# Kernel optimization log

Hardware: AMD Instinct MI355X
Metric: run time of the kernel (lower is better)

The kernel has to match this reference:

```python
import jax, jax.numpy as jnp
import numpy as np

B, NB, NS, C, HID, NP, NH = 8, 2048, 1024, 768, 3072, 1024, 6
HD = C // NH


def _ln(x, w, b):
    mu = x.mean(-1, keepdims=True)
    var = ((x - mu) ** 2).mean(-1, keepdims=True)
    return (x - mu) / jnp.sqrt(var + 1e-5) * w + b


def _gelu(z):
    return jax.nn.gelu(z, approximate=False)  # torch nn.GELU default = exact erf


def setup_inputs() -> dict:
    key = jax.random.key(0)
    ks = jax.random.split(key, 16)
    p = lambda i, shape: (jax.random.normal(ks[i], shape, jnp.float32) * 0.02)
    inp = {
        'x_b': jax.random.normal(ks[0], (B, NB, C), jnp.float32),
        'x_s': jax.random.normal(ks[1], (B, NS, C), jnp.float32),
        # token_types[0,0]=0 -> KV is computed (no stale cache), as on the first call
        'token_types': jax.random.randint(ks[2], (B, NS), 0, 2, jnp.int32).at[0, 0].set(0),
        'base_idxs': jax.random.randint(ks[3], (B, NP), -3, NB).astype(jnp.int32),
        'ln1_w': jnp.ones(C, jnp.float32), 'ln1_b': jnp.zeros(C, jnp.float32),
        'ln2_w': jnp.ones(C, jnp.float32), 'ln2_b': jnp.zeros(C, jnp.float32),
        'ln3_w': jnp.ones(C, jnp.float32), 'ln3_b': jnp.zeros(C, jnp.float32),
        'Wq': p(4, (C, C)), 'Wkv': p(5, (C, 2 * C)),
        'es_w1': p(6, (C, HID)), 'es_b1': jnp.zeros(HID, jnp.float32),
        'es_w2': p(7, (HID, C)), 'es_b2': jnp.zeros(C, jnp.float32),
        'el_w1': p(8, (C, HID)), 'el_b1': jnp.zeros(HID, jnp.float32),
        'el_w2': p(9, (HID, C)), 'el_b2': jnp.zeros(C, jnp.float32),
        'mlp_w1': p(10, (C, 4 * C)), 'mlp_b1': jnp.zeros(4 * C, jnp.float32),
        'mlp_w2': p(11, (4 * C, C)), 'mlp_b2': jnp.zeros(C, jnp.float32),
    }
    return inp


def reference(x_b, x_s, token_types, base_idxs,
              ln1_w, ln1_b, ln2_w, ln2_b, ln3_w, ln3_b,
              Wq, Wkv, es_w1, es_b1, es_w2, es_b2,
              el_w1, el_b1, el_w2, el_b2,
              mlp_w1, mlp_b1, mlp_w2, mlp_b2):
    Bn, Ns, Cd = x_s.shape
    # --- norm1/norm2 + cross-attention (q from x_s, kv from x_b) ---
    xs_n = _ln(x_s, ln1_w, ln1_b)
    xb_n = _ln(x_b, ln2_w, ln2_b)
    q = (xs_n @ Wq).reshape(Bn, Ns, NH, HD).transpose(0, 2, 1, 3)          # (B,H,Ns,hd)
    kv = (xb_n @ Wkv).reshape(Bn, -1, 2, NH, HD).transpose(2, 0, 3, 1, 4)  # (2,B,H,Nb,hd)
    k_, v_ = kv[0], kv[1]
    attn = jax.nn.softmax(jnp.einsum('bhqd,bhkd->bhqk', q, k_) * (HD ** -0.5), axis=-1)
    ctx = jnp.einsum('bhqk,bhkd->bhqd', attn, v_).transpose(0, 2, 1, 3).reshape(Bn, Ns, Cd)
    # --- 2-expert MoE MLP routed by token_types (0 -> expert_s, 1 -> expert_l) ---
    out_s = _gelu(ctx @ es_w1 + es_b1) @ es_w2 + es_b2
    out_l = _gelu(ctx @ el_w1 + el_b1) @ el_w2 + el_b2
    tt = token_types[..., None]
    moe = jnp.where(tt == 0, out_s, 0.0) + jnp.where(tt == 1, out_l, 0.0)
    x = x_s + moe
    # --- residual MLP ---
    x = x + (_gelu(_ln(x, ln3_w, ln3_b) @ mlp_w1 + mlp_b1) @ mlp_w2 + mlp_b2)
    x_norm = x / jnp.maximum(jnp.linalg.norm(x, axis=-1, keepdims=True), 1e-12)
    # --- masked-token kernel (vectorized over batch, masking replaces gather) ---
    nh = base_idxs.shape[1] // 2
    ids = base_idxs[:, :nh]
    mask = ids >= 0                                        # (B,nh)
    idc = jnp.where(mask, ids, 0)
    tokens = jnp.take_along_axis(x_b, idc[:, :, None], axis=1) * mask[..., None]
    sc = jnp.einsum('bic,bjc->bij', tokens, tokens) / jnp.sqrt(jnp.float32(Cd))
    kbias = jnp.where(mask, 0.0, -1e9)[:, None, :]
    aw = jax.nn.softmax(sc + kbias, axis=-1)
    agg = jnp.einsum('bij,bjc->bic', aw, tokens)
    cnt = mask.sum(-1)
    ksum = (agg * mask[..., None]).sum(1) / jnp.maximum(cnt, 1)[:, None]
    kn = ksum / jnp.maximum(jnp.linalg.norm(ksum, axis=-1, keepdims=True), 1e-12)
    has = (cnt > 0)[:, None]
    kernel = jnp.where(has, kn, 0.0)                        # (B,C)
    pos = jnp.where(has, (jnp.einsum('bnc,bc->bn', x_norm, kernel) + 1.0) / 2.0, 0.0)
    # --- top-k selection with data-dependent valid_k and straight-through binarize ---
    kk = Ns // 8
    topv, topi = jax.lax.top_k(pos, kk)
    cnt65 = (pos > 0.65).sum(-1)
    vk = jnp.minimum(kk, jnp.maximum(kk - 10, cnt65))
    keep = jnp.arange(kk)[None, :] < vk[:, None]
    vals = topv * keep
    sel = vals[:, :, None] * jax.nn.one_hot(topi, Ns, dtype=x.dtype)
    binary = (sel > 0.0).astype(x.dtype)
    sel = sel + jax.lax.stop_gradient(binary - sel)
    return sel, topi, pos, x, kernel[:, None, :]
```

## Files before the change

### kernel.cpp

```cpp
#include <hip/hip_runtime.h>
#include <hip/hip_bf16.h>
#include <math.h>

#define B_   8
#define NB_  2048
#define NS_  1024
#define Cc_  768
#define HID_ 3072
#define NP_  1024
#define NH_  6
#define HD_  128

__device__ __forceinline__ float gelu_exact(float v) {
  return 0.5f * v * (1.0f + erff(v * 0.7071067811865476f));
}

__device__ __forceinline__ void split3(float v, unsigned short& h,
                                       unsigned short& m, unsigned short& l) {
  unsigned hb = __float_as_uint(v) & 0xffff0000u;
  float r1 = v - __uint_as_float(hb);
  unsigned mb = __float_as_uint(r1) & 0xffff0000u;
  float r2 = r1 - __uint_as_float(mb);
  unsigned lb = __float_as_uint(r2) & 0xffff0000u;
  h = (unsigned short)(hb >> 16);
  m = (unsigned short)(mb >> 16);
  l = (unsigned short)(lb >> 16);
}

typedef short bf16x8 __attribute__((ext_vector_type(8)));
typedef float f32x4 __attribute__((ext_vector_type(4)));

#define BLOCK_REDUCE_ADD(red, tid)                                              \
  for (int off_ = 128; off_; off_ >>= 1) {                                      \
    if ((tid) < off_) red[(tid)] += red[(tid) + off_];                          \
    __syncthreads();                                                            \
  }

__global__ __launch_bounds__(256) void ln_split(
    const float* __restrict__ x, unsigned short* __restrict__ y,
    const float* __restrict__ w, const float* __restrict__ b) {
  __shared__ float red[256];
  int row = blockIdx.x, tid = threadIdx.x;
  const float* xr = x + (size_t)row * Cc_;
  float v0 = xr[tid], v1 = xr[tid + 256], v2 = xr[tid + 512];
  red[tid] = v0 + v1 + v2;
  __syncthreads();
  BLOCK_REDUCE_ADD(red, tid);
  float mu = red[0] / (float)Cc_;
  __syncthreads();
  float d0 = v0 - mu, d1 = v1 - mu, d2 = v2 - mu;
  red[tid] = d0 * d0 + d1 * d1 + d2 * d2;
  __syncthreads();
  BLOCK_REDUCE_ADD(red, tid);
  float var = red[0] / (float)Cc_;
  float rs = 1.0f / sqrtf(var + 1e-5f);
  unsigned short* yr = y + (size_t)row * 2304;
  float vals[3] = {d0 * rs * w[tid] + b[tid],
                   d1 * rs * w[tid + 256] + b[tid + 256],
                   d2 * rs * w[tid + 512] + b[tid + 512]};
#pragma unroll
  for (int t = 0; t < 3; ++t) {
    int c = tid + (t << 8);
    unsigned short h16, m16, l16;
    split3(vals[t], h16, m16, l16);
    yr[c] = h16; yr[768 + c] = m16; yr[1536 + c] = l16;
  }
}

__global__ __launch_bounds__(256) void split_kernel(
    const float* __restrict__ x, unsigned short* __restrict__ y) {
  size_t idx = (size_t)blockIdx.x * 256 + threadIdx.x;
  int c = (int)(idx % Cc_);
  int row = (int)(idx / Cc_);
  unsigned short h16, m16, l16;
  split3(x[idx], h16, m16, l16);
  unsigned short* yr = y + (size_t)row * 2304;
  yr[c] = h16; yr[768 + c] = m16; yr[1536 + c] = l16;
}

__global__ __launch_bounds__(256) void rownorm_kernel(
    const float* __restrict__ x, float* __restrict__ y) {
  __shared__ float red[256];
  int row = blockIdx.x, tid = threadIdx.x;
  const float* xr = x + (size_t)row * Cc_;
  float* yr = y + (size_t)row * Cc_;
  float v0 = xr[tid], v1 = xr[tid + 256], v2 = xr[tid + 512];
  red[tid] = v0 * v0 + v1 * v1 + v2 * v2;
  __syncthreads();
  BLOCK_REDUCE_ADD(red, tid);
  float den = fmaxf(sqrtf(red[0]), 1e-12f);
  yr[tid]       = v0 / den;
  yr[tid + 256] = v1 / den;
  yr[tid + 512] = v2 / den;
}

__global__ __launch_bounds__(256) void wconv(
    const float* __restrict__ W, unsigned short* __restrict__ out,
    int K, int N, int ldw, int ncol0) {
  int k = blockIdx.x * 256 + threadIdx.x;
  int n = blockIdx.y;
  float v = W[(size_t)k * ldw + ncol0 + n];
  unsigned short h16, m16, l16;
  split3(v, h16, m16, l16);
  size_t base = (size_t)n * 3 * K;
  out[base + k] = h16;
  out[base + K + k] = m16;
  out[base + 2 * K + k] = l16;
}

template <int EPI, bool AGATHER, bool MDEV>
__global__ __launch_bounds__(256) void mgemm(
    const unsigned short* __restrict__ Ap, const unsigned short* __restrict__ Bp,
    float* __restrict__ Cf, unsigned short* __restrict__ Cs,
    const float* __restrict__ bias,
    const int* __restrict__ perm, const int* __restrict__ mdev,
    int M, int N, int K, int ldc, int Kout, int nsplit, long zstride,
    float scale) {
  __shared__ unsigned short As[2][8192];
  __shared__ unsigned short Bs[2][8192];
  int Me = MDEV ? mdev[0] : M;
  int m0 = blockIdx.y * 128, n0 = blockIdx.x * 128;
  if (MDEV && m0 >= Me) return;
  int tid = threadIdx.x;
  int lane = tid & 63, w = tid >> 6;
  int wr = w >> 1, wc = w & 1;
  int K3 = 3 * K;
  int tps = K >> 6;
  int KT = 6 * tps;
  int z = blockIdx.z;
  int span = KT / nsplit;
  int tt0 = z * span, tt1 = tt0 + span;

  const unsigned short* agp[4];
  const unsigned short* bgp[4];
  int wswz[4];
#pragma unroll
  for (int p = 0; p < 4; ++p) {
    int r = (tid >> 3) + 32 * p;
    int ma = m0 + r;
    if (MDEV) ma = min(ma, Me - 1);
    if (AGATHER) ma = perm[ma];
    agp[p] = Ap + (size_t)ma * K3 + (tid & 7) * 8;
    bgp[p] = Bp + (size_t)(n0 + r) * K3 + (tid & 7) * 8;
    wswz[p] = r * 64 + (((tid & 7) ^ (r & 7)) << 3);
  }

  f32x4 acc[4][4];
  f32x4 zero4 = {0.f, 0.f, 0.f, 0.f};
#pragma unroll
  for (int i = 0; i < 4; ++i)
#pragma unroll
    for (int j = 0; j < 4; ++j) acc[i][j] = zero4;

  int kg = lane >> 4;
  int frm[4], frn[4];
#pragma unroll
  for (int f = 0; f < 4; ++f) {
    frm[f] = wr * 64 + f * 16 + (lane & 15);
    frn[f] = wc * 64 + f * 16 + (lane & 15);
  }

  bf16x8 ra[4], rb[4];
  {
    int seg = tt0 / tps, kt = tt0 - seg * tps;
    int pa = (0x210100u >> (4 * seg)) & 0xF;
    int pb = (0x012010u >> (4 * seg)) & 0xF;
    size_t ao = (size_t)(pa * K + kt * 64);
    size_t bo = (size_t)(pb * K + kt * 64);
#pragma unroll
    for (int p = 0; p < 4; ++p) {
      ra[p] = *(const bf16x8*)(agp[p] + ao);
      rb[p] = *(const bf16x8*)(bgp[p] + bo);
    }
  }

  for (int tt = tt0; tt < tt1; ++tt) {
    int cur = tt & 1;
#pragma unroll
    for (int p = 0; p < 4; ++p) {
      *(bf16x8*)&As[cur][wswz[p]] = ra[p];
      *(bf16x8*)&Bs[cur][wswz[p]] = rb[p];
    }
    if (tt + 1 < tt1) {
      int seg = (tt + 1) / tps, kt = (tt + 1) - seg * tps;
      int pa = (0x210100u >> (4 * seg)) & 0xF;
      int pb = (0x012010u >> (4 * seg)) & 0xF;
      size_t ao = (size_t)(pa * K + kt * 64);
      size_t bo = (size_t)(pb * K + kt * 64);
#pragma unroll
      for (int p = 0; p < 4; ++p) {
        ra[p] = *(const bf16x8*)(agp[p] + ao);
        rb[p] = *(const bf16x8*)(bgp[p] + bo);
      }
    }
    asm volatile("s_waitcnt lgkmcnt(0)" ::: "memory");
    __builtin_amdgcn_s_barrier();
#pragma unroll
    for (int ks = 0; ks < 2; ++ks) {
      int ch = ks * 4 + kg;
      bf16x8 af[4], bf[4];
#pragma unroll
      for (int f = 0; f < 4; ++f) {
        int r = frm[f];
        af[f] = *(const bf16x8*)&As[cur][r * 64 + ((ch ^ (r & 7)) << 3)];
      }
#pragma unroll
      for (int f = 0; f < 4; ++f) {
        int r = frn[f];
        bf[f] = *(const bf16x8*)&Bs[cur][r * 64 + ((ch ^ (r & 7)) << 3)];
      }
#pragma unroll
      for (int i = 0; i < 4; ++i)
#pragma unroll
        for (int j = 0; j < 4; ++j)
          acc[i][j] = __builtin_amdgcn_mfma_f32_16x16x32_bf16(
              af[i], bf[j], acc[i][j], 0, 0, 0);
    }
  }

#pragma unroll
  for (int i = 0; i < 4; ++i) {
#pragma unroll
    for (int r = 0; r < 4; ++r) {
      int m = m0 + wr * 64 + i * 16 + kg * 4 + r;
      if (MDEV && m >= Me) continue;
#pragma unroll
      for (int j = 0; j < 4; ++j) {
        int n = n0 + wc * 64 + j * 16 + (lane & 15);
        float v = acc[i][j][r] * scale;
        if (EPI == 6) {
          Cf[(size_t)z * zstride + (size_t)m * ldc + n] = v;
        } else if (EPI == 7) {
          Cf[(size_t)z * zstride + (size_t)m * ldc + n] += v;
        } else if (EPI == 5) {
          float t = gelu_exact(v + bias[n]);
          unsigned short h16, m16, l16;
          split3(t, h16, m16, l16);
          size_t base = (size_t)m * 3 * Kout;
          Cs[base + n] = h16;
          Cs[base + Kout + n] = m16;
          Cs[base + 2 * Kout + n] = l16;
        }
      }
    }
  }
}

template <bool SCATTER>
__global__ __launch_bounds__(256) void combineP(
    const float* __restrict__ P0, const float* __restrict__ P1,
    const float* __restrict__ bias, const float* __restrict__ addsrc,
    const int* __restrict__ perm, const int* __restrict__ cnt,
    float* __restrict__ out) {
  int m = blockIdx.x;
  int c = threadIdx.x + (blockIdx.y << 8);
  if (SCATTER && m >= cnt[0]) return;
  int mo = SCATTER ? perm[m] : m;
  size_t pm = (size_t)m * 768 + c;
  out[(size_t)mo * 768 + c] =
      bias[c] + addsrc[(size_t)mo * 768 + c] + P0[pm] + P1[pm];
}

template <int EPI, int TRB, bool AGATHER, bool MDEV>
__global__ __launch_bounds__(256) void gemm128(
    const float* __restrict__ A, const float* __restrict__ Bm,
    float* __restrict__ Cm, const float* __restrict__ bias,
    const float* __restrict__ addsrc, const int* __restrict__ perm,
    const int* __restrict__ mdev,
    int M, int N, int K, int lda, int ldb, int ldc,
    int d1, int d2,
    long a_s1, long a_s2, long a_s3,
    long b_s1, long b_s2, long b_s3,
    long c_s1, long c_s2, long c_s3,
    float scale) {
  __shared__ float As[2][16][132];
  __shared__ float Bs[2][16][132];
  int z = blockIdx.z;
  int z1 = z / (d1 * d2);
  int rem = z - z1 * d1 * d2;
  int z2 = rem / d2, z3 = rem - z2 * d2;
  const float* Ab = A + (size_t)z1 * a_s1 + (size_t)z2 * a_s2 + (size_t)z3 * a_s3;
  const float* Bb = Bm + (size_t)z1 * b_s1 + (size_t)z2 * b_s2 + (size_t)z3 * b_s3;
  float* Cb = Cm + (size_t)z1 * c_s1 + (size_t)z2 * c_s2 + (size_t)z3 * c_s3;
  int Me = MDEV ? mdev[0] : M;
  int m0 = blockIdx.y * 128, n0 = blockIdx.x * 128;
  if (MDEV && m0 >= Me) return;
  int tid = threadIdx.x;
  int tx = tid & 15, ty = tid >> 4;
  int arow = tid >> 2, akq = tid & 3;
  int ma0 = m0 + arow, ma1 = m0 + arow + 64;
  if (MDEV) { ma0 = min(ma0, Me - 1); ma1 = min(ma1, Me - 1); }
  if (AGATHER) { ma0 = perm[ma0]; ma1 = perm[ma1]; }
  const float* Ap0 = Ab + (size_t)ma0 * lda + akq * 4;
  const float* Ap1 = Ab + (size_t)ma1 * lda + akq * 4;
  const float* Bp0;
  const float* Bp1;
  int bw_r0 = 0, bw_c0 = 0, bw_r1 = 0;
  if (TRB == 0) {
    bw_r0 = tid >> 5; bw_c0 = (tid & 31) * 4; bw_r1 = bw_r0 + 8;
    Bp0 = Bb + (size_t)bw_r0 * ldb + n0 + bw_c0;
    Bp1 = Bb + (size_t)bw_r1 * ldb + n0 + bw_c0;
  } else {
    Bp0 = Bb + (size_t)(n0 + arow) * ldb + akq * 4;
    Bp1 = Bb + (size_t)(n0 + arow + 64) * ldb + akq * 4;
  }
  float4 pa0 = *(const float4*)Ap0;
  float4 pa1 = *(const float4*)Ap1;
  float4 pb0 = *(const float4*)Bp0;
  float4 pb1 = *(const float4*)Bp1;
  float acc[8][8] = {};
  int nt = K >> 4;
  for (int t = 0; t < nt; ++t) {
    int cur = t & 1;
    As[cur][akq * 4 + 0][arow] = pa0.x; As[cur][akq * 4 + 1][arow] = pa0.y;
    As[cur][akq * 4 + 2][arow] = pa0.z; As[cur][akq * 4 + 3][arow] = pa0.w;
    As[cur][akq * 4 + 0][arow + 64] = pa1.x; As[cur][akq * 4 + 1][arow + 64] = pa1.y;
    As[cur][akq * 4 + 2][arow + 64] = pa1.z; As[cur][akq * 4 + 3][arow + 64] = pa1.w;
    if (TRB == 0) {
      *(float4*)&Bs[cur][bw_r0][bw_c0] = pb0;
      *(float4*)&Bs[cur][bw_r1][bw_c0] = pb1;
    } else {
      Bs[cur][akq * 4 + 0][arow] = pb0.x; Bs[cur][akq * 4 + 1][arow] = pb0.y;
      Bs[cur][akq * 4 + 2][arow] = pb0.z; Bs[cur][akq * 4 + 3][arow] = pb0.w;
      Bs[cur][akq * 4 + 0][arow + 64] = pb1.x; Bs[cur][akq * 4 + 1][arow + 64] = pb1.y;
      Bs[cur][akq * 4 + 2][arow + 64] = pb1.z; Bs[cur][akq * 4 + 3][arow + 64] = pb1.w;
    }
    if (t + 1 < nt) {
      int kn = (t + 1) << 4;
      pa0 = *(const float4*)&Ap0[kn];
      pa1 = *(const float4*)&Ap1[kn];
      if (TRB == 0) {
        pb0 = *(const float4*)&Bp0[(size_t)kn * ldb];
        pb1 = *(const float4*)&Bp1[(size_t)kn * ldb];
      } else {
        pb0 = *(const float4*)&Bp0[kn];
        pb1 = *(const float4*)&Bp1[kn];
      }
    }
    asm volatile("s_waitcnt lgkmcnt(0)" ::: "memory");
    __builtin_amdgcn_s_barrier();
#pragma unroll
    for (int kk = 0; kk < 16; ++kk) {
      float a[8], b[8];
      *(float4*)&a[0] = *(const float4*)&As[cur][kk][ty * 4];
      *(float4*)&a[4] = *(const float4*)&As[cur][kk][ty * 4 + 64];
      *(float4*)&b[0] = *(const float4*)&Bs[cur][kk][tx * 4];
      *(float4*)&b[4] = *(const float4*)&Bs[cur][kk][tx * 4 + 64];
#pragma unroll
      for (int i = 0; i < 8; ++i)
#pragma unroll
        for (int j = 0; j < 8; ++j)
          acc[i][j] = fmaf(a[i], b[j], acc[i][j]);
    }
  }
#pragma unroll
  for (int i = 0; i < 8; ++i) {
    int m = m0 + ((i < 4) ? (ty * 4 + i) : (64 + ty * 4 + i - 4));
    if (!MDEV || m < Me) {
      int mo = (EPI == 4) ? perm[m] : m;
      int n = n0 + tx * 4;
      float v[8];
#pragma unroll
      for (int j = 0; j < 8; ++j) {
        int nj = (j < 4) ? (n + j) : (n + 64 + j - 4);
        v[j] = acc[i][j] * scale;
        if (EPI >= 1) v[j] += bias[nj];
        if (EPI == 2) v[j] = gelu_exact(v[j]);
        if (EPI == 3 || EPI == 4) v[j] += addsrc[(size_t)mo * ldc + nj];
      }
      float* cp = &Cb[(size_t)mo * ldc + n];
      *(float4*)cp = make_float4(v[0], v[1], v[2], v[3]);
      *(float4*)(cp + 64) = make_float4(v[4], v[5], v[6], v[7]);
    }
  }
}

__global__ __launch_bounds__(256) void pv_reduce(
    const float* __restrict__ part, float* __restrict__ ctx) {
  int i = blockIdx.x * 256 + threadIdx.x;
  int n = i & 127, m = (i >> 7) & 1023, h = i >> 17;
  float s = 0.f;
#pragma unroll
  for (int ks = 0; ks < 16; ++ks)
    s += part[(size_t)(ks * 6 + h) * 131072 + m * 128 + n];
  ctx[(size_t)m * 768 + h * 128 + n] = s;
}

template <int EPT, bool MASK>
__global__ __launch_bounds__(256) void softmax_kernel(
    float* __restrict__ s, const float* __restrict__ maskf) {
  __shared__ float red[256];
  int row = blockIdx.x, tid = threadIdx.x;
  float* sr = s + (size_t)row * (EPT * 256);
  const float* mb = MASK ? (maskf + (size_t)(row / 512) * 512) : nullptr;
  float v[EPT];
  float m = -3.0e38f;
#pragma unroll
  for (int t = 0; t < EPT; ++t) {
    int j = tid + (t << 8);
    float xv = sr[j];
    if (MASK) xv += (mb[j] != 0.0f) ? 0.0f : -1e9f;
    v[t] = xv;
    m = fmaxf(m, xv);
  }
  red[tid] = m;
  __syncthreads();
  for (int off = 128; off; off >>= 1) {
    if (tid < off) red[tid] = fmaxf(red[tid], red[tid + off]);
    __syncthreads();
  }
  m = red[0];
  __syncthreads();
  float ssum = 0.f;
#pragma unroll
  for (int t = 0; t < EPT; ++t) {
    v[t] = expf(v[t] - m);
    ssum += v[t];
  }
  red[tid] = ssum;
  __syncthreads();
  BLOCK_REDUCE_ADD(red, tid);
  float tot = red[0];
#pragma unroll
  for (int t = 0; t < EPT; ++t) sr[tid + (t << 8)] = v[t] / tot;
}

__global__ __launch_bounds__(256) void build_perm(
    const int* __restrict__ tt, int* __restrict__ perm0,
    int* __restrict__ perm1, int* __restrict__ cnt) {
  int r = blockIdx.x * 256 + threadIdx.x;
  int t = tt[r];
  if (t == 0) { int p = atomicAdd(&cnt[0], 1); perm0[p] = r; }
  else        { int p = atomicAdd(&cnt[1], 1); perm1[p] = r; }
}

__global__ __launch_bounds__(256) void gather_kernel(
    const float* __restrict__ xb, const int* __restrict__ bidx,
    float* __restrict__ tokens, float* __restrict__ maskf) {
  size_t idx = (size_t)blockIdx.x * 256 + threadIdx.x;
  int c = (int)(idx % Cc_);
  int i = (int)((idx / Cc_) % 512);
  int b = (int)(idx / ((size_t)Cc_ * 512));
  int id = bidx[b * NP_ + i];
  bool m = id >= 0;
  int idc = m ? id : 0;
  tokens[idx] = m ? xb[((size_t)b * NB_ + idc) * Cc_ + c] : 0.0f;
  if (c == 0) maskf[b * 512 + i] = m ? 1.0f : 0.0f;
}

__global__ __launch_bounds__(256) void kernel_kernel(
    const float* __restrict__ agg, const float* __restrict__ maskf,
    float* __restrict__ kern, float* __restrict__ hasf) {
  __shared__ float red[256];
  __shared__ float ks[Cc_];
  __shared__ float s_cnt;
  int b = blockIdx.x, tid = threadIdx.x;
  const float* mb = maskf + b * 512;
  red[tid] = mb[tid] + mb[tid + 256];
  __syncthreads();
  BLOCK_REDUCE_ADD(red, tid);
  if (tid == 0) s_cnt = red[0];
  __syncthreads();
  float cnt = s_cnt;
  float dc = fmaxf(cnt, 1.0f);
  const float* ab = agg + (size_t)b * 512 * Cc_;
#pragma unroll
  for (int t = 0; t < 3; ++t) {
    int cc = tid + t * 256;
    float s = 0.f;
    for (int i = 0; i < 512; ++i) s = fmaf(ab[(size_t)i * Cc_ + cc], mb[i], s);
    ks[cc] = s / dc;
  }
  __syncthreads();
  float s2 = 0.f;
#pragma unroll
  for (int t = 0; t < 3; ++t) {
    float q = ks[tid + t * 256];
    s2 = fmaf(q, q, s2);
  }
  red[tid] = s2;
  __syncthreads();
  BLOCK_REDUCE_ADD(red, tid);
  float den = fmaxf(sqrtf(red[0]), 1e-12f);
  bool has = cnt > 0.5f;
#pragma unroll
  for (int t = 0; t < 3; ++t) {
    int cc = tid + t * 256;
    kern[(size_t)b * Cc_ + cc] = has ? (ks[cc] / den) : 0.0f;
  }
  if (tid == 0) hasf[b] = has ? 1.0f : 0.0f;
}

__global__ __launch_bounds__(256) void pos_kernel(
    const float* __restrict__ xnorm, const float* __restrict__ kern,
    const float* __restrict__ hasf, float* __restrict__ pos) {
  __shared__ float red[256];
  int row = blockIdx.x, tid = threadIdx.x;
  int b = row >> 10;
  const float* xr = xnorm + (size_t)row * Cc_;
  const float* kr = kern + (size_t)b * Cc_;
  float s = xr[tid] * kr[tid];
  s = fmaf(xr[tid + 256], kr[tid + 256], s);
  s = fmaf(xr[tid + 512], kr[tid + 512], s);
  red[tid] = s;
  __syncthreads();
  BLOCK_REDUCE_ADD(red, tid);
  if (tid == 0) pos[row] = (hasf[b] > 0.5f) ? (red[0] + 1.0f) * 0.5f : 0.0f;
}

__global__ __launch_bounds__(256) void topk_kernel(
    const float* __restrict__ pos, float* __restrict__ sel,
    float* __restrict__ topi) {
  __shared__ float vals[NS_];
  __shared__ float rv[256];
  __shared__ int ri[256];
  __shared__ int s_vk;
  int b = blockIdx.x, tid = threadIdx.x;
  const float* pr = pos + (size_t)b * NS_;
  int c65 = 0;
#pragma unroll
  for (int t = 0; t < 4; ++t) {
    float v = pr[tid + (t << 8)];
    vals[tid + (t << 8)] = v;
    if (v > 0.65f) ++c65;
  }
  ri[tid] = c65;
  __syncthreads();
  for (int off = 128; off; off >>= 1) {
    if (tid < off) ri[tid] += ri[tid + off];
    __syncthreads();
  }
  if (tid == 0) {
    int vk = ri[0] > 118 ? ri[0] : 118;
    s_vk = vk > 128 ? 128 : vk;
  }
  __syncthreads();
  int vk = s_vk;
  for (int r = 0; r < 128; ++r) {
    float bv = -3.0e38f;
    int bi = 0x7fffffff;
#pragma unroll
    for (int t = 0; t < 4; ++t) {
      int i = tid + (t << 8);
      float v = vals[i];
      if (v > bv) { bv = v; bi = i; }
    }
    rv[tid] = bv; ri[tid] = bi;
    __syncthreads();
    for (int off = 128; off; off >>= 1) {
      if (tid < off) {
        float ov = rv[tid + off]; int oi = ri[tid + off];
        if (ov > rv[tid] || (ov == rv[tid] && oi < ri[tid])) {
          rv[tid] = ov; ri[tid] = oi;
        }
      }
      __syncthreads();
    }
    if (tid == 0) {
      int wi = ri[0]; float wv = rv[0];
      topi[(size_t)b * 128 + r] = (float)wi;
      if (r < vk && wv > 0.0f) sel[((size_t)b * 128 + r) * NS_ + wi] = 1.0f;
      vals[wi] = -3.0e38f;
    }
    __syncthreads();
  }
}

extern "C" void kernel_launch(void* const* d_in, const int* in_sizes, int n_in,
                              void* d_out, int out_size, void* d_ws, size_t ws_size,
                              hipStream_t stream) {
  (void)in_sizes; (void)n_in; (void)out_size; (void)ws_size;
  const float* x_b = (const float*)d_in[0];
  const float* x_s = (const float*)d_in[1];
  const int* token_types = (const int*)d_in[2];
  const int* base_idxs = (const int*)d_in[3];
  const float* ln1_w = (const float*)d_in[4];
  const float* ln1_b = (const float*)d_in[5];
  const float* ln2_w = (const float*)d_in[6];
  const float* ln2_b = (const float*)d_in[7];
  const float* ln3_w = (const float*)d_in[8];
  const float* ln3_b = (const float*)d_in[9];
  const float* Wq = (const float*)d_in[10];
  const float* Wkv = (const float*)d_in[11];
  const float* es_w1 = (const float*)d_in[12];
  const float* es_b1 = (const float*)d_in[13];
  const float* es_w2 = (const float*)d_in[14];
  const float* es_b2 = (const float*)d_in[15];
  const float* el_w1 = (const float*)d_in[16];
  const float* el_b1 = (const float*)d_in[17];
  const float* el_w2 = (const float*)d_in[18];
  const float* el_b2 = (const float*)d_in[19];
  const float* mlp_w1 = (const float*)d_in[20];
  const float* mlp_b1 = (const float*)d_in[21];
  const float* mlp_w2 = (const float*)d_in[22];
  const float* mlp_b2 = (const float*)d_in[23];

  float* out = (float*)d_out;
  float* sel_out  = out;
  float* topi_out = out + 1048576;
  float* pos_out  = out + 1049600;
  float* x_out    = out + 1057792;
  float* kern_out = out + 7349248;

  float* w = (float*)d_ws;
  float* q_f  = w;
  float* kv_f = w + 6291456;
  unsigned short* xbnp = (unsigned short*)(w + 31457280);
  unsigned short* xsnp = (unsigned short*)(w + 50331648);
  unsigned short* wqp  = (unsigned short*)(w + 59768832);
  unsigned short* wkvp = wqp + 1769472;
  float* scores = w + 31457280;
  float* part   = w + 44040192;
  float* ctxf   = w + 56623104;
  unsigned short* ctxp = (unsigned short*)(w + 6291456);
  unsigned short* wb   = (unsigned short*)(w + 15728640);
  unsigned short* hp   = (unsigned short*)(w + 36962304);
  float* P0 = w;
  const long ZS = 55836672;
  float* P1 = w + ZS;
  float* xn     = w + 6291456;
  float* tokens = w + 12582912;
  float* aw     = w + 15728640;
  float* agg    = w + 17825792;
  float* small  = w + 62914560;
  float* maskf  = small;
  float* hasf   = small + 4096;
  int* cnt      = (int*)(small + 4104);
  int* perm0    = (int*)(small + 4106);
  int* perm1    = (int*)(small + 12298);

  unsigned short* esw1h[2] = {wb + 0,        wb + 3538944};
  unsigned short* elw1h[2] = {wb + 7077888,  wb + 10616832};
  unsigned short* mlw1h[2] = {wb + 14155776, wb + 17694720};
  unsigned short* esw2h[2] = {wb + 21233664, wb + 24772608};
  unsigned short* elw2h[2] = {wb + 28311552, wb + 31850496};
  unsigned short* mlw2h[2] = {wb + 35389440, wb + 38928384};

  const long NSC = (long)NS_ * Cc_;
  const long NB2C = (long)NB_ * 2 * Cc_;
  const long SNB = (long)NS_ * NB_;
  const float qk_scale = 0.08838834764831845f;
  const float sc_scale = 0.036084391824351615f;

  hipMemsetAsync(sel_out, 0, (size_t)1048576 * sizeof(float), stream);
  hipMemsetAsync(cnt, 0, 2 * sizeof(int), stream);

  ln_split<<<B_ * NS_, 256, 0, stream>>>(x_s, xsnp, ln1_w, ln1_b);
  ln_split<<<B_ * NB_, 256, 0, stream>>>(x_b, xbnp, ln2_w, ln2_b);
  build_perm<<<32, 256, 0, stream>>>(token_types, perm0, perm1, cnt);
  wconv<<<dim3(3, 768), 256, 0, stream>>>(Wq, wqp, 768, 768, 768, 0);
  wconv<<<dim3(3, 1536), 256, 0, stream>>>(Wkv, wkvp, 768, 1536, 1536, 0);
  mgemm<6, false, false><<<dim3(6, 64, 1), 256, 0, stream>>>(
      xsnp, wqp, q_f, nullptr, nullptr, nullptr, nullptr,
      8192, 768, 768, 768, 0, 1, 0, 1.0f);
  mgemm<6, false, false><<<dim3(12, 128, 1), 256, 0, stream>>>(
      xbnp, wkvp, kv_f, nullptr, nullptr, nullptr, nullptr,
      16384, 1536, 768, 1536, 0, 1, 0, 1.0f);

  for (int b = 0; b < B_; ++b) {
    const float* qb = q_f + (size_t)b * NSC;
    const float* kb = kv_f + (size_t)b * NB2C;
    const float* vb = kb + Cc_;
    gemm128<0, 1, false, false><<<dim3(16, 8, 6), 256, 0, stream>>>(
        qb, kb, scores, nullptr, nullptr, nullptr, nullptr,
        1024, 2048, 128, 768, 1536, 2048,
        1, 1, 128, 0, 0, 128, 0, 0, SNB, 0, 0, qk_scale);
    softmax_kernel<8, false><<<6 * 1024, 256, 0, stream>>>(scores, nullptr);
    gemm128<0, 0, false, false><<<dim3(1, 8, 96), 256, 0, stream>>>(
        scores, vb, part, nullptr, nullptr, nullptr, nullptr,
        1024, 128, 128, 2048, 1536, 128,
        6, 16, 0, SNB, 128, 0, 128, 128 * 1536, 0, 131072, 786432, 1.0f);
    pv_reduce<<<3072, 256, 0, stream>>>(part, ctxf + (size_t)b * NSC);
  }

  split_kernel<<<24576, 256, 0, stream>>>(ctxf, ctxp);
  for (int h = 0; h < 2; ++h) {
    wconv<<<dim3(3, 1536), 256, 0, stream>>>(es_w1, esw1h[h], 768, 1536, 3072, h * 1536);
    wconv<<<dim3(3, 1536), 256, 0, stream>>>(el_w1, elw1h[h], 768, 1536, 3072, h * 1536);
    wconv<<<dim3(3, 1536), 256, 0, stream>>>(mlp_w1, mlw1h[h], 768, 1536, 3072, h * 1536);
    wconv<<<dim3(6, 768), 256, 0, stream>>>(es_w2 + (size_t)h * 1536 * 768, esw2h[h], 1536, 768, 768, 0);
    wconv<<<dim3(6, 768), 256, 0, stream>>>(el_w2 + (size_t)h * 1536 * 768, elw2h[h], 1536, 768, 768, 0);
    wconv<<<dim3(6, 768), 256, 0, stream>>>(mlp_w2 + (size_t)h * 1536 * 768, mlw2h[h], 1536, 768, 768, 0);
  }

  for (int h = 0; h < 2; ++h) {
    mgemm<5, true, true><<<dim3(12, 64, 1), 256, 0, stream>>>(
        ctxp, esw1h[h], nullptr, hp, es_b1 + h * 1536, perm0, cnt,
        8192, 1536, 768, 0, 1536, 1, 0, 1.0f);
    if (h == 0)
      mgemm<6, false, true><<<dim3(6, 64, 2), 256, 0, stream>>>(
          hp, esw2h[h], P0, nullptr, nullptr, nullptr, cnt,
          8192, 768, 1536, 768, 0, 2, ZS, 1.0f);
    else
      mgemm<7, false, true><<<dim3(6, 64, 2), 256, 0, stream>>>(
          hp, esw2h[h], P0, nullptr, nullptr, nullptr, cnt,
          8192, 768, 1536, 768, 0, 2, ZS, 1.0f);
  }
  combineP<true><<<dim3(8192, 3), 256, 0, stream>>>(
      P0, P1, es_b2, x_s, perm0, cnt, x_out);
  for (int h = 0; h < 2; ++h) {
    mgemm<5, true, true><<<dim3(12, 64, 1), 256, 0, stream>>>(
        ctxp, elw1h[h], nullptr, hp, el_b1 + h * 1536, perm1, cnt + 1,
        8192, 1536, 768, 0, 1536, 1, 0, 1.0f);
    if (h == 0)
      mgemm<6, false, true><<<dim3(6, 64, 2), 256, 0, stream>>>(
          hp, elw2h[h], P0, nullptr, nullptr, nullptr, cnt + 1,
          8192, 768, 1536, 768, 0, 2, ZS, 1.0f);
    else
      mgemm<7, false, true><<<dim3(6, 64, 2), 256, 0, stream>>>(
          hp, elw2h[h], P0, nullptr, nullptr, nullptr, cnt + 1,
          8192, 768, 1536, 768, 0, 2, ZS, 1.0f);
  }
  combineP<true><<<dim3(8192, 3), 256, 0, stream>>>(
      P0, P1, el_b2, x_s, perm1, cnt + 1, x_out);
  ln_split<<<B_ * NS_, 256, 0, stream>>>(x_out, ctxp, ln3_w, ln3_b);
  for (int h = 0; h < 2; ++h) {
    mgemm<5, false, false><<<dim3(12, 64, 1), 256, 0, stream>>>(
        ctxp, mlw1h[h], nullptr, hp, mlp_b1 + h * 1536, nullptr, nullptr,
        8192, 1536, 768, 0, 1536, 1, 0, 1.0f);
    if (h == 0)
      mgemm<6, false, false><<<dim3(6, 64, 2), 256, 0, stream>>>(
          hp, mlw2h[h], P0, nullptr, nullptr, nullptr, nullptr,
          8192, 768, 1536, 768, 0, 2, ZS, 1.0f);
    else
      mgemm<7, false, false><<<dim3(6, 64, 2), 256, 0, stream>>>(
          hp, mlw2h[h], P0, nullptr, nullptr, nullptr, nullptr,
          8192, 768, 1536, 768, 0, 2, ZS, 1.0f);
  }
  combineP<false><<<dim3(8192, 3), 256, 0, stream>>>(
      P0, P1, mlp_b2, x_out, nullptr, nullptr, x_out);

  rownorm_kernel<<<B_ * NS_, 256, 0, stream>>>(x_out, xn);
  gather_kernel<<<12288, 256, 0, stream>>>(x_b, base_idxs, tokens, maskf);
  gemm128<0, 1, false, false><<<dim3(4, 4, 8), 256, 0, stream>>>(
      tokens, tokens, aw, nullptr, nullptr, nullptr, nullptr,
      512, 512, 768, 768, 768, 512,
      1, 1, 393216, 0, 0, 393216, 0, 0, 262144, 0, 0, sc_scale);
  softmax_kernel<2, true><<<8 * 512, 256, 0, stream>>>(aw, maskf);
  gemm128<0, 0, false, false><<<dim3(6, 4, 8), 256, 0, stream>>>(
      aw, tokens, agg, nullptr, nullptr, nullptr, nullptr,
      512, 768, 512, 512, 768, 768,
      1, 1, 262144, 0, 0, 393216, 0, 0, 393216, 0, 0, 1.0f);
  kernel_kernel<<<8, 256, 0, stream>>>(agg, maskf, kern_out, hasf);
  pos_kernel<<<B_ * NS_, 256, 0, stream>>>(xn, kern_out, hasf, pos_out);
  topk_kernel<<<8, 256, 0, stream>>>(pos_out, sel_out, topi_out);
}
```

Before: 3.416 ms.

## Run QK^T scores on split-bf16 matrix-core GEMM and halve PV split-K

The per-batch attention score GEMM moves from the fp32 gemm128 path to the split-bf16 (3-way) mgemm matrix-core kernel. New qsplit/ksplit kernels convert Q and K per head into the split layout first. mgemm gains per-z A/B strides and a block-id swizzle that remaps tiles across groups of eight blocks, probably for cache locality. The PV split-K is halved from 16 to 8 chunks, so pv_reduce has fewer partials to sum, at the cost of less parallelism per GEMM and extra split-conversion launches per batch.

```diff
diff --git a/kernel.cpp b/kernel.cpp
--- a/kernel.cpp
+++ b/kernel.cpp
@@ -76,6 +76,28 @@
   split3(x[idx], h16, m16, l16);
   unsigned short* yr = y + (size_t)row * 2304;
   yr[c] = h16; yr[768 + c] = m16; yr[1536 + c] = l16;
+}
+
+__global__ __launch_bounds__(256) void qsplit(
+    const float* __restrict__ q, unsigned short* __restrict__ qp) {
+  int idx = blockIdx.x * 256 + threadIdx.x;
+  int c = idx & 127, m = (idx >> 7) & 1023, h = idx >> 17;
+  float v = q[(size_t)m * 768 + h * 128 + c];
+  unsigned short h16, m16, l16;
+  split3(v, h16, m16, l16);
+  size_t base = (size_t)h * 393216 + (size_t)m * 384;
+  qp[base + c] = h16; qp[base + 128 + c] = m16; qp[base + 256 + c] = l16;
+}
+
+__global__ __launch_bounds__(256) void ksplit(
+    const float* __restrict__ kv, unsigned short* __restrict__ kp) {
+  int idx = blockIdx.x * 256 + threadIdx.x;
+  int c = idx & 127, n = (idx >> 7) & 2047, h = idx >> 18;
+  float v = kv[(size_t)n * 1536 + h * 128 + c];
+  unsigned short h16, m16, l16;
+  split3(v, h16, m16, l16);
+  size_t base = (size_t)h * 786432 + (size_t)n * 384;
+  kp[base + c] = h16; kp[base + 128 + c] = m16; kp[base + 256 + c] = l16;
 }
 
 __global__ __launch_bounds__(256) void rownorm_kernel(
@@ -114,22 +136,30 @@
     float* __restrict__ Cf, unsigned short* __restrict__ Cs,
     const float* __restrict__ bias,
     const int* __restrict__ perm, const int* __restrict__ mdev,
-    int M, int N, int K, int ldc, int Kout, int nsplit, long zstride,
-    float scale) {
+    int M, int N, int K, int ldc, int Kout, int nsplit,
+    long azs, long bzs, long zstride, float scale) {
   __shared__ unsigned short As[2][8192];
   __shared__ unsigned short Bs[2][8192];
+  int z = blockIdx.z;
+  int gx = gridDim.x;
+  int id = blockIdx.y * gx + blockIdx.x;
+  int per = (gx * gridDim.y) >> 3;
+  int nid = (id & 7) * per + (id >> 3);
+  int bx = nid % gx, by = nid / gx;
   int Me = MDEV ? mdev[0] : M;
-  int m0 = blockIdx.y * 128, n0 = blockIdx.x * 128;
+  int m0 = by * 128, n0 = bx * 128;
   if (MDEV && m0 >= Me) return;
+  const unsigned short* ApB = Ap + (size_t)z * azs;
+  const unsigned short* BpB = Bp + (size_t)z * bzs;
   int tid = threadIdx.x;
   int lane = tid & 63, w = tid >> 6;
   int wr = w >> 1, wc = w & 1;
   int K3 = 3 * K;
   int tps = K >> 6;
   int KT = 6 * tps;
-  int z = blockIdx.z;
   int span = KT / nsplit;
-  int tt0 = z * span, tt1 = tt0 + span;
+  int zr = z % nsplit;
+  int tt0 = zr * span, tt1 = tt0 + span;
 
   const unsigned short* agp[4];
   const unsigned short* bgp[4];
@@ -140,8 +170,8 @@
     int ma = m0 + r;
     if (MDEV) ma = min(ma, Me - 1);
     if (AGATHER) ma = perm[ma];
-    agp[p] = Ap + (size_t)ma * K3 + (tid & 7) * 8;
-    bgp[p] = Bp + (size_t)(n0 + r) * K3 + (tid & 7) * 8;
+    agp[p] = ApB + (size_t)ma * K3 + (tid & 7) * 8;
+    bgp[p] = BpB + (size_t)(n0 + r) * K3 + (tid & 7) * 8;
     wswz[p] = r * 64 + (((tid & 7) ^ (r & 7)) << 3);
   }
 
@@ -381,7 +411,7 @@
   int n = i & 127, m = (i >> 7) & 1023, h = i >> 17;
   float s = 0.f;
 #pragma unroll
-  for (int ks = 0; ks < 16; ++ks)
+  for (int ks = 0; ks < 8; ++ks)
     s += part[(size_t)(ks * 6 + h) * 131072 + m * 128 + n];
   ctx[(size_t)m * 768 + h * 128 + n] = s;
 }
@@ -603,15 +633,17 @@
   float* kern_out = out + 7349248;
 
   float* w = (float*)d_ws;
-  float* q_f  = w;
-  float* kv_f = w + 6291456;
+  float* kv_f = w;
+  float* q_f  = w + 25165824;
+  float* scores = w + 31457280;
+  float* part   = w + 44040192;
+  float* ctxf   = w + 50331648;
+  unsigned short* qp_b = (unsigned short*)(w + 56623104);
+  unsigned short* kp_b = (unsigned short*)(w + 57802752);
   unsigned short* xbnp = (unsigned short*)(w + 31457280);
   unsigned short* xsnp = (unsigned short*)(w + 50331648);
   unsigned short* wqp  = (unsigned short*)(w + 59768832);
-  unsigned short* wkvp = wqp + 1769472;
-  float* scores = w + 31457280;
-  float* part   = w + 44040192;
-  float* ctxf   = w + 56623104;
+  unsigned short* wkvp = (unsigned short*)(w + 60653568);
   unsigned short* ctxp = (unsigned short*)(w + 6291456);
   unsigned short* wb   = (unsigned short*)(w + 15728640);
   unsigned short* hp   = (unsigned short*)(w + 36962304);
@@ -652,24 +684,25 @@
   wconv<<<dim3(3, 1536), 256, 0, stream>>>(Wkv, wkvp, 768, 1536, 1536, 0);
   mgemm<6, false, false><<<dim3(6, 64, 1), 256, 0, stream>>>(
       xsnp, wqp, q_f, nullptr, nullptr, nullptr, nullptr,
-      8192, 768, 768, 768, 0, 1, 0, 1.0f);
+      8192, 768, 768, 768, 0, 1, 0, 0, 0, 1.0f);
   mgemm<6, false, false><<<dim3(12, 128, 1), 256, 0, stream>>>(
       xbnp, wkvp, kv_f, nullptr, nullptr, nullptr, nullptr,
-      16384, 1536, 768, 1536, 0, 1, 0, 1.0f);
+      16384, 1536, 768, 1536, 0, 1, 0, 0, 0, 1.0f);
 
   for (int b = 0; b < B_; ++b) {
     const float* qb = q_f + (size_t)b * NSC;
-    const float* kb = kv_f + (size_t)b * NB2C;
-    const float* vb = kb + Cc_;
-    gemm128<0, 1, false, false><<<dim3(16, 8, 6), 256, 0, stream>>>(
-        qb, kb, scores, nullptr, nullptr, nullptr, nullptr,
-        1024, 2048, 128, 768, 1536, 2048,
-        1, 1, 128, 0, 0, 128, 0, 0, SNB, 0, 0, qk_scale);
+    const float* kvb = kv_f + (size_t)b * NB2C;
+    const float* vb = kvb + Cc_;
+    qsplit<<<3072, 256, 0, stream>>>(qb, qp_b);
+    ksplit<<<6144, 256, 0, stream>>>(kvb, kp_b);
+    mgemm<6, false, false><<<dim3(16, 8, 6), 256, 0, stream>>>(
+        qp_b, kp_b, scores, nullptr, nullptr, nullptr, nullptr,
+        1024, 2048, 128, 2048, 0, 1, 393216, 786432, SNB, qk_scale);
     softmax_kernel<8, false><<<6 * 1024, 256, 0, stream>>>(scores, nullptr);
-    gemm128<0, 0, false, false><<<dim3(1, 8, 96), 256, 0, stream>>>(
+    gemm128<0, 0, false, false><<<dim3(1, 8, 48), 256, 0, stream>>>(
         scores, vb, part, nullptr, nullptr, nullptr, nullptr,
-        1024, 128, 128, 2048, 1536, 128,
-        6, 16, 0, SNB, 128, 0, 128, 128 * 1536, 0, 131072, 786432, 1.0f);
+        1024, 128, 256, 2048, 1536, 128,
+        6, 8, 0, SNB, 256, 0, 128, 393216, 0, 131072, 786432, 1.0f);
     pv_reduce<<<3072, 256, 0, stream>>>(part, ctxf + (size_t)b * NSC);
   }
 
@@ -686,30 +719,30 @@
   for (int h = 0; h < 2; ++h) {
     mgemm<5, true, true><<<dim3(12, 64, 1), 256, 0, stream>>>(
         ctxp, esw1h[h], nullptr, hp, es_b1 + h * 1536, perm0, cnt,
-        8192, 1536, 768, 0, 1536, 1, 0, 1.0f);
+        8192, 1536, 768, 0, 1536, 1, 0, 0, 0, 1.0f);
     if (h == 0)
       mgemm<6, false, true><<<dim3(6, 64, 2), 256, 0, stream>>>(
           hp, esw2h[h], P0, nullptr, nullptr, nullptr, cnt,
-          8192, 768, 1536, 768, 0, 2, ZS, 1.0f);
+          8192, 768, 1536, 768, 0, 2, 0, 0, ZS, 1.0f);
     else
       mgemm<7, false, true><<<dim3(6, 64, 2), 256, 0, stream>>>(
           hp, esw2h[h], P0, nullptr, nullptr, nullptr, cnt,
-          8192, 768, 1536, 768, 0, 2, ZS, 1.0f);
+          8192, 768, 1536, 768, 0, 2, 0, 0, ZS, 1.0f);
   }
   combineP<true><<<dim3(8192, 3), 256, 0, stream>>>(
       P0, P1, es_b2, x_s, perm0, cnt, x_out);
   for (int h = 0; h < 2; ++h) {
     mgemm<5, true, true><<<dim3(12, 64, 1), 256, 0, stream>>>(
         ctxp, elw1h[h], nullptr, hp, el_b1 + h * 1536, perm1, cnt + 1,
-        8192, 1536, 768, 0, 1536, 1, 0, 1.0f);
+        8192, 1536, 768, 0, 1536, 1, 0, 0, 0, 1.0f);
     if (h == 0)
       mgemm<6, false, true><<<dim3(6, 64, 2), 256, 0, stream>>>(
           hp, elw2h[h], P0, nullptr, nullptr, nullptr, cnt + 1,
-          8192, 768, 1536, 768, 0, 2, ZS, 1.0f);
+          8192, 768, 1536, 768, 0, 2, 0, 0, ZS, 1.0f);
     else
       mgemm<7, false, true><<<dim3(6, 64, 2), 256, 0, stream>>>(
           hp, elw2h[h], P0, nullptr, nullptr, nullptr, cnt + 1,
-          8192, 768, 1536, 768, 0, 2, ZS, 1.0f);
+          8192, 768, 1536, 768, 0, 2, 0, 0, ZS, 1.0f);
   }
   combineP<true><<<dim3(8192, 3), 256, 0, stream>>>(
       P0, P1, el_b2, x_s, perm1, cnt + 1, x_out);
@@ -717,15 +750,15 @@
   for (int h = 0; h < 2; ++h) {
     mgemm<5, false, false><<<dim3(12, 64, 1), 256, 0, stream>>>(
         ctxp, mlw1h[h], nullptr, hp, mlp_b1 + h * 1536, nullptr, nullptr,
-        8192, 1536, 768, 0, 1536, 1, 0, 1.0f);
+        8192, 1536, 768, 0, 1536, 1, 0, 0, 0, 1.0f);
     if (h == 0)
       mgemm<6, false, false><<<dim3(6, 64, 2), 256, 0, stream>>>(
           hp, mlw2h[h], P0, nullptr, nullptr, nullptr, nullptr,
-          8192, 768, 1536, 768, 0, 2, ZS, 1.0f);
+          8192, 768, 1536, 768, 0, 2, 0, 0, ZS, 1.0f);
     else
       mgemm<7, false, false><<<dim3(6, 64, 2), 256, 0, stream>>>(
           hp, mlw2h[h], P0, nullptr, nullptr, nullptr, nullptr,
-          8192, 768, 1536, 768, 0, 2, ZS, 1.0f);
+          8192, 768, 1536, 768, 0, 2, 0, 0, ZS, 1.0f);
   }
   combineP<false><<<dim3(8192, 3), 256, 0, stream>>>(
       P0, P1, mlp_b2, x_out, nullptr, nullptr, x_out);
```

New measurement: 3.725 ms. 9.0% more time.
